# Kernel tuning notes

Measured on AMD Instinct MI355X. Metric: run time of the kernel, lower is better.

The kernel has to match this reference:

```python
import jax, jax.numpy as jnp
import numpy as np

U = 400000   # num users
I = 400000   # num items
D = 64       # dim_each_feedback
B = 2        # num behaviors in this feedback group
E = 2000000  # edges per behavior


def setup_inputs() -> dict:
    key = jax.random.key(0)
    ks = jax.random.split(key, 7)
    return {
        "user_emb": jax.random.normal(ks[0], (U, D), jnp.float32) * 0.1,
        "item_emb": jax.random.normal(ks[1], (I, D), jnp.float32) * 0.1,
        "u_w": jax.random.normal(ks[2], (D, D), jnp.float32) * (1.0 / np.sqrt(D)),
        "i_w": jax.random.normal(ks[3], (D, D), jnp.float32) * (1.0 / np.sqrt(D)),
        "vals": jax.random.uniform(ks[4], (B, E), jnp.float32),
        "rows": jax.random.randint(ks[5], (B, E), 0, U),   # user index of each edge
        "cols": jax.random.randint(ks[6], (B, E), 0, I),   # item index of each edge
    }


def _spmm(vals, idx_src, idx_dst, x, n_out):
    # y = A @ x where sparse A has A[idx_dst, idx_src] = vals (COO).
    # Equivalent to torch.spmm over the concatenation of row-wise folds.
    msg = vals[:, None] * x[idx_src]                       # [E, D]
    return jax.ops.segment_sum(msg, idx_dst, num_segments=n_out)


def reference(user_emb, item_emb, u_w, i_w, vals, rows, cols):
    # Per-behavior aggregation (folds concatenated == full spmm per behavior)
    u_agg = jax.vmap(lambda v, r, c: _spmm(v, c, r, item_emb, U))(vals, rows, cols)  # [B,U,D]
    i_agg = jax.vmap(lambda v, r, c: _spmm(v, r, c, user_emb, I))(vals, rows, cols)  # [B,I,D]
    user_embedding = jax.nn.sigmoid(jnp.mean(u_agg, axis=0) @ u_w)   # [U,D]
    item_embedding = jax.nn.sigmoid(jnp.mean(i_agg, axis=0) @ i_w)   # [I,D]
    user_embeddings = jax.nn.sigmoid(u_agg @ u_w)                    # [B,U,D]
    item_embeddings = jax.nn.sigmoid(i_agg @ i_w)                    # [B,I,D]
    return (user_embedding, item_embedding, user_embeddings, item_embeddings)
```

## Files before the change

kernel.cpp:

```cpp
#include <hip/hip_runtime.h>

#define U_N 400000
#define I_N 400000
#define DD  64
#define BB  2
#define EE  2000000


__global__ __launch_bounds__(128) void rowgemm(const float* __restrict__ X,
                                               const float* __restrict__ Wm,
                                               float* __restrict__ Y, int n) {
    __shared__ float xs[2][64][65];
    const int wv = threadIdx.x >> 6;
    const int ln = threadIdx.x & 63;
    const int rowbase = blockIdx.x * 128 + wv * 64;

    for (int m = 0; m < 16; ++m) {
        int f  = m * 64 + ln;
        int r  = f >> 4, c4 = f & 15;
        long gr = rowbase + r; if (gr >= n) gr = n - 1;
        float4 v = ((const float4*)X)[gr * 16 + c4];
        xs[wv][r][c4 * 4 + 0] = v.x;
        xs[wv][r][c4 * 4 + 1] = v.y;
        xs[wv][r][c4 * 4 + 2] = v.z;
        xs[wv][r][c4 * 4 + 3] = v.w;
    }
    __syncthreads();

    float acc[64];
#pragma unroll
    for (int j = 0; j < 64; ++j) acc[j] = 0.f;

    for (int k = 0; k < 64; ++k) {
        float xv = xs[wv][ln][k];
#pragma unroll
        for (int j = 0; j < 64; ++j)
            acc[j] = fmaf(xv, Wm[k * 64 + j], acc[j]);
    }

    int row = rowbase + ln;
    if (row < n) {
#pragma unroll
        for (int q = 0; q < 16; ++q) {
            float4 v = make_float4(acc[4*q], acc[4*q+1], acc[4*q+2], acc[4*q+3]);
            ((float4*)Y)[(long)row * 16 + q] = v;
        }
    }
}

__global__ __launch_bounds__(256) void scatter(const float* __restrict__ twI,
                                               const float* __restrict__ twU,
                                               const float* __restrict__ vals,
                                               const int*   __restrict__ rows,
                                               const int*   __restrict__ cols,
                                               float* __restrict__ uT,
                                               float* __restrict__ iT) {
    const int total16 = BB * EE * 16;
    int tid    = blockIdx.x * blockDim.x + threadIdx.x;
    int stride = gridDim.x * blockDim.x;
    for (int t = tid; t < total16; t += stride) {
        int g = t >> 4;
        int q = t & 15;
        float val = vals[g];
        int u  = rows[g];
        int it = cols[g];
        int b  = (g >= EE) ? 1 : 0;

        float4 xv = ((const float4*)twI)[(long)it * 16 + q];
        float4 yv = ((const float4*)twU)[(long)u  * 16 + q];

        float* ud = uT + ((long)b * U_N + u)  * 64 + q * 4;
        float* id = iT + ((long)b * I_N + it) * 64 + q * 4;

        unsafeAtomicAdd(ud + 0, val * xv.x);
        unsafeAtomicAdd(ud + 1, val * xv.y);
        unsafeAtomicAdd(ud + 2, val * xv.z);
        unsafeAtomicAdd(ud + 3, val * xv.w);

        unsafeAtomicAdd(id + 0, val * yv.x);
        unsafeAtomicAdd(id + 1, val * yv.y);
        unsafeAtomicAdd(id + 2, val * yv.z);
        unsafeAtomicAdd(id + 3, val * yv.w);
    }
}

__device__ __forceinline__ float sig(float x) { return 1.f / (1.f + expf(-x)); }
__device__ __forceinline__ float4 sig4(float4 v) {
    return make_float4(sig(v.x), sig(v.y), sig(v.z), sig(v.w));
}

__global__ __launch_bounds__(256) void epilogue(float* __restrict__ out) {
    const int UD4 = U_N * DD / 4;
    float4* o4 = (float4*)out;
    int tid    = blockIdx.x * blockDim.x + threadIdx.x;
    int stride = gridDim.x * blockDim.x;
    for (int t = tid; t < 2 * UD4; t += stride) {
        int side = (t >= UD4) ? 1 : 0;
        int idx  = t - side * UD4;
        long tb  = 2L * UD4 + (long)side * 2 * UD4 + idx;
        float4 t0 = o4[tb];
        float4 t1 = o4[tb + UD4];
        float4 tm = make_float4(0.5f * (t0.x + t1.x), 0.5f * (t0.y + t1.y),
                                0.5f * (t0.z + t1.z), 0.5f * (t0.w + t1.w));
        o4[tb]        = sig4(t0);
        o4[tb + UD4]  = sig4(t1);
        o4[(long)side * UD4 + idx] = sig4(tm);
    }
}

extern "C" void kernel_launch(void* const* d_in, const int* in_sizes, int n_in,
                              void* d_out, int out_size, void* d_ws, size_t ws_size,
                              hipStream_t stream) {
    const float* user_emb = (const float*)d_in[0];
    const float* item_emb = (const float*)d_in[1];
    const float* u_w      = (const float*)d_in[2];
    const float* i_w      = (const float*)d_in[3];
    const float* vals     = (const float*)d_in[4];
    const int*   rows     = (const int*)  d_in[5];
    const int*   cols     = (const int*)  d_in[6];

    float* out = (float*)d_out;
    const long UD = (long)U_N * DD;
    float* tw_item = out;
    float* tw_user = out + UD;
    float* uT      = out + 2 * UD;
    float* iT      = out + 2 * UD + (long)BB * UD;

    hipMemsetAsync(uT, 0, (size_t)2 * BB * UD * sizeof(float), stream);

    rowgemm<<<(I_N + 127) / 128, 128, 0, stream>>>(item_emb, u_w, tw_item, I_N);
    rowgemm<<<(U_N + 127) / 128, 128, 0, stream>>>(user_emb, i_w, tw_user, U_N);

    scatter<<<16384, 256, 0, stream>>>(tw_item, tw_user, vals, rows, cols, uT, iT);

    epilogue<<<8192, 256, 0, stream>>>(out);
}
```

Measured before the change: 7.787 ms.

## Replace atomic scatter with counting-sort CSR build and per-row gather accumulation

```diff
diff --git a/kernel.cpp b/kernel.cpp
--- a/kernel.cpp
+++ b/kernel.cpp
@@ -48,6 +48,69 @@
     }
 }
 
+__global__ __launch_bounds__(256) void hist_kernel(const int* __restrict__ idx,
+                                                   int* __restrict__ counts) {
+    int tid = blockIdx.x * blockDim.x + threadIdx.x;
+    int stride = gridDim.x * blockDim.x;
+    for (int e = tid; e < EE; e += stride) atomicAdd(&counts[idx[e]], 1);
+}
+
+#define SCAN_T 1024
+__global__ __launch_bounds__(SCAN_T) void scan_kernel(const int* __restrict__ counts,
+                                                      int* __restrict__ base,
+                                                      int* __restrict__ cursor, int n) {
+    __shared__ int ssum[SCAN_T];
+    const int ch = (n + SCAN_T - 1) / SCAN_T;
+    int t = threadIdx.x;
+    int lo = t * ch; int hi = min(lo + ch, n);
+    int s = 0;
+    for (int i = lo; i < hi; ++i) s += counts[i];
+    ssum[t] = s; __syncthreads();
+    for (int off = 1; off < SCAN_T; off <<= 1) {
+        int v = (t >= off) ? ssum[t - off] : 0;
+        __syncthreads();
+        ssum[t] += v;
+        __syncthreads();
+    }
+    int run = ssum[t] - s;
+    for (int i = lo; i < hi; ++i) {
+        int c = counts[i];
+        base[i] = run; cursor[i] = run; run += c;
+    }
+}
+
+__global__ __launch_bounds__(256) void place_kernel(const int* __restrict__ idx,
+                                                    const int* __restrict__ src,
+                                                    const float* __restrict__ vals,
+                                                    int* __restrict__ cursor,
+                                                    float2* __restrict__ payload) {
+    int tid = blockIdx.x * blockDim.x + threadIdx.x;
+    int stride = gridDim.x * blockDim.x;
+    for (int e = tid; e < EE; e += stride) {
+        int d = idx[e];
+        int p = atomicAdd(&cursor[d], 1);
+        payload[p] = make_float2(vals[e], __int_as_float(src[e]));
+    }
+}
+
+__global__ __launch_bounds__(256) void accum_kernel(const float2* __restrict__ payload,
+                                                    const int* __restrict__ base,
+                                                    const int* __restrict__ counts,
+                                                    const float* __restrict__ tw,
+                                                    float* __restrict__ outp, int n) {
+    int wid  = (blockIdx.x * blockDim.x + threadIdx.x) >> 6;
+    int lane = threadIdx.x & 63;
+    if (wid >= n) return;
+    int st = base[wid], cnt = counts[wid];
+    float acc = 0.f;
+    for (int k = 0; k < cnt; ++k) {
+        float2 p = payload[st + k];
+        int s = __float_as_int(p.y);
+        acc += p.x * tw[(long)s * 64 + lane];
+    }
+    outp[(long)wid * 64 + lane] = acc;
+}
+
 __global__ __launch_bounds__(256) void scatter(const float* __restrict__ twI,
                                                const float* __restrict__ twU,
                                                const float* __restrict__ vals,
@@ -65,18 +128,14 @@
         int u  = rows[g];
         int it = cols[g];
         int b  = (g >= EE) ? 1 : 0;
-
         float4 xv = ((const float4*)twI)[(long)it * 16 + q];
         float4 yv = ((const float4*)twU)[(long)u  * 16 + q];
-
         float* ud = uT + ((long)b * U_N + u)  * 64 + q * 4;
         float* id = iT + ((long)b * I_N + it) * 64 + q * 4;
-
         unsafeAtomicAdd(ud + 0, val * xv.x);
         unsafeAtomicAdd(ud + 1, val * xv.y);
         unsafeAtomicAdd(ud + 2, val * xv.z);
         unsafeAtomicAdd(ud + 3, val * xv.w);
-
         unsafeAtomicAdd(id + 0, val * yv.x);
         unsafeAtomicAdd(id + 1, val * yv.y);
         unsafeAtomicAdd(id + 2, val * yv.z);
@@ -126,12 +185,34 @@
     float* uT      = out + 2 * UD;
     float* iT      = out + 2 * UD + (long)BB * UD;
 
-    hipMemsetAsync(uT, 0, (size_t)2 * BB * UD * sizeof(float), stream);
-
     rowgemm<<<(I_N + 127) / 128, 128, 0, stream>>>(item_emb, u_w, tw_item, I_N);
     rowgemm<<<(U_N + 127) / 128, 128, 0, stream>>>(user_emb, i_w, tw_user, U_N);
 
-    scatter<<<16384, 256, 0, stream>>>(tw_item, tw_user, vals, rows, cols, uT, iT);
+    const size_t need = (size_t)3 * 400000 * sizeof(int) + (size_t)EE * sizeof(float2);
+    if (ws_size >= need) {
+        int*    counts  = (int*)d_ws;
+        int*    base    = counts + 400000;
+        int*    cursor  = base   + 400000;
+        float2* payload = (float2*)(cursor + 400000);
+
+        for (int pass = 0; pass < 4; ++pass) {
+            int dir = pass >> 1, b = pass & 1;
+            const int*   idx = (dir == 0 ? rows : cols) + (long)b * EE;
+            const int*   sr  = (dir == 0 ? cols : rows) + (long)b * EE;
+            const float* vv  = vals + (long)b * EE;
+            const float* tw  = dir == 0 ? tw_item : tw_user;
+            float*       op  = (dir == 0 ? uT : iT) + (long)b * U_N * DD;
+
+            hipMemsetAsync(counts, 0, 400000 * sizeof(int), stream);
+            hist_kernel <<<2048, 256, 0, stream>>>(idx, counts);
+            scan_kernel <<<1, SCAN_T, 0, stream>>>(counts, base, cursor, 400000);
+            place_kernel<<<2048, 256, 0, stream>>>(idx, sr, vv, cursor, payload);
+            accum_kernel<<<100000, 256, 0, stream>>>(payload, base, counts, tw, op, 400000);
+        }
+    } else {
+        hipMemsetAsync(uT, 0, (size_t)2 * BB * UD * sizeof(float), stream);
+        scatter<<<16384, 256, 0, stream>>>(tw_item, tw_user, vals, rows, cols, uT, iT);
+    }
 
     epilogue<<<8192, 256, 0, stream>>>(out);
 }
```

New measurement: 6.581 ms. 1.18x faster.
